# Optimization experiments

Measured on AMD Instinct MI355X. Metric: run time of the kernel, lower is better.

## Reference

```python
import jax, jax.numpy as jnp
import numpy as np

# Static multi-scale feature map shapes (value_spatial_shapes) - constants for jit.
SPATIAL = [(128, 128), (64, 64), (32, 32), (16, 16)]
D = 256      # embed_dim
NH = 8       # num_heads
HD = D // NH # head_dim = 32
L = 4        # num_levels
P = 4        # num_points
TP = NH * L * P  # 128 total points


def setup_inputs() -> dict:
    key = jax.random.key(0)
    ks = jax.random.split(key, 10)
    bs, lq = 8, 300
    lv = sum(h * w for h, w in SPATIAL)  # 21760
    s = D ** -0.5
    return {
        "query": jax.random.normal(ks[0], (bs, lq, D), jnp.float32),
        "reference_points": jax.random.uniform(ks[1], (bs, lq, L, 4), jnp.float32),
        "value": jax.random.normal(ks[2], (bs, lv, D), jnp.float32),
        "W_value": jax.random.normal(ks[3], (D, D), jnp.float32) * s,
        "b_value": jnp.zeros((D,), jnp.float32),
        "W_off": jax.random.normal(ks[4], (D, TP * 2), jnp.float32) * (s * 0.01),
        "b_off": jax.random.normal(ks[5], (TP * 2,), jnp.float32) * 0.5,
        "W_attn": jax.random.normal(ks[6], (D, TP), jnp.float32) * (s * 0.01),
        "b_attn": jnp.zeros((TP,), jnp.float32),
        "W_out": jax.random.normal(ks[7], (D, D), jnp.float32) * s,
        "b_out": jnp.zeros((D,), jnp.float32),
    }


def _grid_sample(img, grid):
    """torch F.grid_sample(mode='bilinear', padding_mode='zeros', align_corners=False).
    img: [N, C, H, W]; grid: [N, Hg, Wg, 2] in [-1, 1] (x, y). Returns [N, C, Hg, Wg]."""
    N, C, H, W = img.shape
    gx = (grid[..., 0] + 1.0) * (W * 0.5) - 0.5
    gy = (grid[..., 1] + 1.0) * (H * 0.5) - 0.5
    x0f = jnp.floor(gx)
    y0f = jnp.floor(gy)
    x0 = x0f.astype(jnp.int32)
    y0 = y0f.astype(jnp.int32)
    x1, y1 = x0 + 1, y0 + 1
    wx1 = gx - x0f
    wy1 = gy - y0f
    wx0 = 1.0 - wx1
    wy0 = 1.0 - wy1
    imgf = img.reshape(N, C, H * W)

    def gather(ix, iy):
        valid = (ix >= 0) & (ix < W) & (iy >= 0) & (iy < H)
        idx = jnp.clip(iy, 0, H - 1) * W + jnp.clip(ix, 0, W - 1)
        v = jax.vmap(lambda im, ii: im[:, ii])(imgf, idx)  # [N, C, Hg, Wg]
        return v * valid[:, None, :, :].astype(img.dtype)

    return (gather(x0, y0) * (wx0 * wy0)[:, None]
            + gather(x1, y0) * (wx1 * wy0)[:, None]
            + gather(x0, y1) * (wx0 * wy1)[:, None]
            + gather(x1, y1) * (wx1 * wy1)[:, None])


def reference(query, reference_points, value, W_value, b_value, W_off, b_off,
              W_attn, b_attn, W_out, b_out):
    bs, lq, _ = query.shape
    # value projection + head split
    v = (value @ W_value + b_value).reshape(bs, -1, NH, HD)
    # sampling offsets and attention weights from query
    off = (query @ W_off + b_off).reshape(bs, lq, NH, L, P, 2)
    aw = jax.nn.softmax((query @ W_attn + b_attn).reshape(bs, lq, NH, L * P), axis=-1)
    aw = aw.reshape(bs, lq, NH, L, P)
    # reference_points last dim == 4 branch (cx, cy, w, h)
    ref = reference_points  # [bs, lq, L, 4]
    loc = ref[:, :, None, :, None, :2] + off / P * ref[:, :, None, :, None, 2:] * 0.5
    grids = 2.0 * loc - 1.0  # [bs, lq, NH, L, P, 2]
    # split value per level
    splits = np.cumsum([h * w for h, w in SPATIAL])[:-1]
    v_list = jnp.split(v, splits, axis=1)
    samples = []
    for l, (h, w) in enumerate(SPATIAL):
        img = v_list[l].transpose(0, 2, 3, 1).reshape(bs * NH, HD, h, w)
        g = grids[:, :, :, l].transpose(0, 2, 1, 3, 4).reshape(bs * NH, lq, P, 2)
        samples.append(_grid_sample(img, g))  # [bs*NH, HD, lq, P]
    samp = jnp.stack(samples, axis=-2).reshape(bs * NH, HD, lq, L * P)
    awr = aw.transpose(0, 2, 1, 3, 4).reshape(bs * NH, 1, lq, L * P)
    out = (samp * awr).sum(-1).reshape(bs, NH * HD, lq).transpose(0, 2, 1)
    return out @ W_out + b_out
```

## Files before the change

kernel.cpp:

```cpp
#include <hip/hip_runtime.h>
#include <hip/hip_bf16.h>

typedef short bf16x8 __attribute__((ext_vector_type(8)));
typedef unsigned short u16x8 __attribute__((ext_vector_type(8)));
typedef float f32x4 __attribute__((ext_vector_type(4)));

#define LQ 300
#define LV 21760
#define NQ 2400
#define MROWS 174080

#define VBM 32
#define VGRID 512
#define QBLK 38
#define VNT (MROWS / VBM)

__device__ __forceinline__ unsigned short f2bf(float x) {
    __hip_bfloat16 h = __float2bfloat16(x);
    return *reinterpret_cast<unsigned short*>(&h);
}
__device__ __forceinline__ float bf2f(unsigned short s) {
    return __uint_as_float(((unsigned)s) << 16);
}
__device__ __forceinline__ bf16x8 cvt8(float4 a, float4 b) {
    u16x8 u;
    u[0] = f2bf(a.x); u[1] = f2bf(a.y); u[2] = f2bf(a.z); u[3] = f2bf(a.w);
    u[4] = f2bf(b.x); u[5] = f2bf(b.y); u[6] = f2bf(b.z); u[7] = f2bf(b.w);
    return (bf16x8)u;
}
__device__ __forceinline__ bf16x8 cvt8v(f32x4 a, f32x4 b) {
    u16x8 u;
    u[0] = f2bf(a[0]); u[1] = f2bf(a[1]); u[2] = f2bf(a[2]); u[3] = f2bf(a[3]);
    u[4] = f2bf(b[0]); u[5] = f2bf(b[1]); u[6] = f2bf(b[2]); u[7] = f2bf(b[3]);
    return (bf16x8)u;
}

__global__ void k_wt(const float* __restrict__ Wv, const float* __restrict__ Woff,
                     const float* __restrict__ Wattn, const float* __restrict__ Wout,
                     unsigned short* __restrict__ ws) {
    int i = blockIdx.x * 256 + threadIdx.x;
    if (i < 65536) {
        int n = i >> 8, k = i & 255;
        ws[i] = f2bf(Wv[k * 256 + n]);
    } else if (i < 65536 + 98304) {
        int j = i - 65536;
        int n = j >> 8, k = j & 255;
        float s = (n < 256) ? Woff[k * 256 + n] : Wattn[k * 128 + (n - 256)];
        ws[i] = f2bf(s);
    } else {
        int j = i - 163840;
        int n = j >> 8, k = j & 255;
        ws[i] = f2bf(Wout[k * 256 + n]);
    }
}

__global__ __launch_bounds__(256, 2) void k_vgemm(
    const float* __restrict__ A, const unsigned short* __restrict__ Bt,
    const float* __restrict__ bias, unsigned short* __restrict__ V,
    const float* __restrict__ Q, const unsigned short* __restrict__ Woa,
    const float* __restrict__ b_off, const float* __restrict__ b_attn,
    float* __restrict__ offattn)
{
    __shared__ __align__(16) float buf[2][VBM * 256];
    const int t = threadIdx.x;
    const int lane = t & 63;
    const int wv = t >> 6;
    const int fr = lane & 15, kg = lane >> 4;

    if (blockIdx.x < QBLK) {
        const int rowBase = blockIdx.x * 64;
        int rr[4];
#pragma unroll
        for (int m = 0; m < 4; ++m) rr[m] = min(rowBase + m * 16 + fr, NQ - 1);

        f32x4 acc[4][6];
#pragma unroll
        for (int m = 0; m < 4; m++)
#pragma unroll
            for (int n = 0; n < 6; n++) { f32x4 z = {0.f, 0.f, 0.f, 0.f}; acc[m][n] = z; }

#pragma unroll
        for (int kk = 0; kk < 8; ++kk) {
            const int kb = kk * 32 + kg * 8;
            bf16x8 a[4];
#pragma unroll
            for (int m = 0; m < 4; ++m) {
                float4 q0 = *(const float4*)(Q + (size_t)rr[m] * 256 + kb);
                float4 q1 = *(const float4*)(Q + (size_t)rr[m] * 256 + kb + 4);
                a[m] = cvt8(q0, q1);
            }
#pragma unroll
            for (int n = 0; n < 6; n++) {
                bf16x8 bb = *(const bf16x8*)(Woa + (size_t)(wv * 96 + n * 16 + fr) * 256 + kb);
#pragma unroll
                for (int m = 0; m < 4; ++m)
                    acc[m][n] = __builtin_amdgcn_mfma_f32_16x16x32_bf16(a[m], bb, acc[m][n], 0, 0, 0);
            }
        }

#pragma unroll
        for (int m = 0; m < 4; m++) {
#pragma unroll
            for (int n = 0; n < 6; n++) {
                int col = wv * 96 + n * 16 + fr;
                float bvv = (col < 256) ? b_off[col] : b_attn[col - 256];
#pragma unroll
                for (int r = 0; r < 4; r++) {
                    int row = rowBase + m * 16 + kg * 4 + r;
                    if (row < NQ) offattn[(size_t)row * 384 + col] = acc[m][n][r] + bvv;
                }
            }
        }
        return;
    }

    bf16x8 bw[8][4];
#pragma unroll
    for (int kk = 0; kk < 8; ++kk)
#pragma unroll
        for (int n = 0; n < 4; ++n)
            bw[kk][n] = *(const bf16x8*)(Bt + (size_t)(wv * 64 + n * 16 + fr) * 256 + kk * 32 + kg * 8);
    float bv[4];
#pragma unroll
    for (int n = 0; n < 4; ++n) bv[n] = bias[wv * 64 + n * 16 + fr];

#define VSTAGE(tile, cb)                                                                  \
    {                                                                                     \
        const char* tb = (const char*)(A + (size_t)(tile) * (VBM * 256));                 \
        _Pragma("unroll")                                                                 \
        for (int i = 0; i < 8; ++i) {                                                     \
            const int r = wv * 8 + i;                                                     \
            __builtin_amdgcn_global_load_lds(                                             \
                (const __attribute__((address_space(1))) void*)                           \
                    (tb + (size_t)r * 1024 + ((lane * 16) ^ ((r & 7) << 4))),             \
                (__attribute__((address_space(3))) void*)&buf[cb][r * 256], 16, 0, 0);    \
        }                                                                                 \
    }

    const int tb0 = (int)blockIdx.x - QBLK;
    VSTAGE(tb0, 0);

    int cur = 0;
    for (int tile = tb0; tile < VNT; tile += VGRID, cur ^= 1) {
        const int nxt = tile + VGRID;
        const bool stged = (nxt < VNT);
        if (stged) VSTAGE(nxt, cur ^ 1);
        if (tile == tb0) {
            if (stged) asm volatile("s_waitcnt vmcnt(8)" ::: "memory");
            else       asm volatile("s_waitcnt vmcnt(0)" ::: "memory");
        } else {
            if (stged) asm volatile("s_waitcnt vmcnt(12)" ::: "memory");
            else       asm volatile("s_waitcnt vmcnt(4)" ::: "memory");
        }
        __builtin_amdgcn_s_barrier();

        const float* lp = buf[cur];
        f32x4 acc[2][4];
#pragma unroll
        for (int m = 0; m < 2; ++m)
#pragma unroll
            for (int n = 0; n < 4; ++n) { f32x4 z = {0.f, 0.f, 0.f, 0.f}; acc[m][n] = z; }

#pragma unroll
        for (int kk = 0; kk < 8; ++kk) {
            bf16x8 a[2];
#pragma unroll
            for (int m = 0; m < 2; ++m) {
                const int row = m * 16 + fr;
                const int bsw = ((kk * 32 + kg * 8) * 4) ^ ((row & 7) << 4);
                f32x4 af0 = *(const f32x4*)((const char*)(lp + row * 256) + bsw);
                f32x4 af1 = *(const f32x4*)((const char*)(lp + row * 256) + (bsw ^ 16));
                a[m] = cvt8v(af0, af1);
            }
#pragma unroll
            for (int m = 0; m < 2; ++m)
#pragma unroll
                for (int n = 0; n < 4; ++n)
                    acc[m][n] = __builtin_amdgcn_mfma_f32_16x16x32_bf16(a[m], bw[kk][n], acc[m][n], 0, 0, 0);
        }

        __builtin_amdgcn_s_barrier();

        unsigned short* cp = (unsigned short*)buf[cur];
#pragma unroll
        for (int n = 0; n < 4; ++n)
#pragma unroll
            for (int m = 0; m < 2; ++m)
#pragma unroll
                for (int r = 0; r < 4; ++r)
                    cp[(m * 16 + kg * 4 + r) * 264 + wv * 64 + n * 16 + fr] =
                        f2bf(acc[m][n][r] + bv[n]);
        asm volatile("s_waitcnt lgkmcnt(0)" ::: "memory");
        __builtin_amdgcn_sched_barrier(0);
        __builtin_amdgcn_s_barrier();

        unsigned short* ob = V + (size_t)tile * (VBM * 256);
#pragma unroll
        for (int i = 0; i < 4; ++i) {
            const int f = i * 256 + t;
            const int row = f >> 5, col = (f & 31) * 8;
            *(u16x8*)(ob + row * 256 + col) = *(const u16x8*)&cp[row * 264 + col];
        }
        __builtin_amdgcn_s_barrier();
    }
#undef VSTAGE
}

__global__ __launch_bounds__(256) void k_sample(
    const float* __restrict__ refp, const float* __restrict__ offattn,
    const unsigned short* __restrict__ V, const unsigned short* __restrict__ Wout,
    const float* __restrict__ b_out, float* __restrict__ out)
{
    __shared__ float aw[2][128], gx[2][128], gy[2][128];
    __shared__ float att_s[2][256];
    const int t = threadIdx.x;
    const int jj = t >> 7;
    const int tt = t & 127;
    const int row = blockIdx.x * 2 + jj;
    const int b = row / LQ;
    const float* oa = offattn + (size_t)row * 384;

    {
        float logit = oa[256 + tt];
        float m = logit;
        m = fmaxf(m, __shfl_xor(m, 1));
        m = fmaxf(m, __shfl_xor(m, 2));
        m = fmaxf(m, __shfl_xor(m, 4));
        m = fmaxf(m, __shfl_xor(m, 8));
        float e = __expf(logit - m);
        float s = e;
        s += __shfl_xor(s, 1);
        s += __shfl_xor(s, 2);
        s += __shfl_xor(s, 4);
        s += __shfl_xor(s, 8);
        aw[jj][tt] = e / s;
        const int l = (tt >> 2) & 3;
        const float Wl = (l == 0) ? 128.f : (l == 1) ? 64.f : (l == 2) ? 32.f : 16.f;
        float ox = oa[2 * tt], oy = oa[2 * tt + 1];
        const float* rp = refp + ((size_t)row * 4 + l) * 4;
        gx[jj][tt] = (rp[0] + ox * 0.125f * rp[2]) * Wl - 0.5f;
        gy[jj][tt] = (rp[1] + oy * 0.125f * rp[3]) * Wl - 0.5f;
    }
    __syncthreads();

    const int h = tt >> 4;
    const int ch = h * 32 + (tt & 15) * 2;
    float acc0 = 0.f, acc1 = 0.f;
#pragma unroll 4
    for (int p = 0; p < 16; p++) {
        const int l = p >> 2;
        const int Wl = (l == 0) ? 128 : (l == 1) ? 64 : (l == 2) ? 32 : 16;
        const int S  = (l == 0) ? 0 : (l == 1) ? 16384 : (l == 2) ? 20480 : 21504;
        int pt = h * 16 + p;
        float a  = aw[jj][pt];
        float sx = gx[jj][pt], sy = gy[jj][pt];
        float x0f = floorf(sx), y0f = floorf(sy);
        int   x0 = (int)x0f, y0 = (int)y0f;
        float wx1 = sx - x0f, wy1 = sy - y0f;
        float wx0 = 1.f - wx1, wy0 = 1.f - wy1;
        bool vx0 = (unsigned)x0 < (unsigned)Wl;
        bool vx1 = (unsigned)(x0 + 1) < (unsigned)Wl;
        bool vy0 = (unsigned)y0 < (unsigned)Wl;
        bool vy1 = (unsigned)(y0 + 1) < (unsigned)Wl;
        float p00x = 0.f, p00y = 0.f, p01x = 0.f, p01y = 0.f;
        float p10x = 0.f, p10y = 0.f, p11x = 0.f, p11y = 0.f;
        size_t pixBase = (size_t)b * LV + S;
        if (vy0) {
            size_t rb = (pixBase + (size_t)y0 * Wl) * 256 + ch;
            if (vx0) { unsigned u = *(const unsigned*)(V + rb + (size_t)x0 * 256);
                       p00x = bf2f((unsigned short)u); p00y = bf2f((unsigned short)(u >> 16)); }
            if (vx1) { unsigned u = *(const unsigned*)(V + rb + (size_t)x0 * 256 + 256);
                       p01x = bf2f((unsigned short)u); p01y = bf2f((unsigned short)(u >> 16)); }
        }
        if (vy1) {
            size_t rb = (pixBase + (size_t)(y0 + 1) * Wl) * 256 + ch;
            if (vx0) { unsigned u = *(const unsigned*)(V + rb + (size_t)x0 * 256);
                       p10x = bf2f((unsigned short)u); p10y = bf2f((unsigned short)(u >> 16)); }
            if (vx1) { unsigned u = *(const unsigned*)(V + rb + (size_t)x0 * 256 + 256);
                       p11x = bf2f((unsigned short)u); p11y = bf2f((unsigned short)(u >> 16)); }
        }
        acc0 += a * (wy0 * (wx0 * p00x + wx1 * p01x) + wy1 * (wx0 * p10x + wx1 * p11x));
        acc1 += a * (wy0 * (wx0 * p00y + wx1 * p01y) + wy1 * (wx0 * p10y + wx1 * p11y));
    }
    att_s[jj][ch] = acc0;
    att_s[jj][ch + 1] = acc1;
    __syncthreads();

    const size_t r0 = (size_t)blockIdx.x * 2;
    float o0 = b_out[t], o1 = o0;
    const unsigned short* wrow = Wout + (size_t)t * 256;
#pragma unroll 8
    for (int k = 0; k < 256; k += 8) {
        bf16x8 w8 = *(const bf16x8*)(wrow + k);
#pragma unroll
        for (int e = 0; e < 8; ++e) {
            float w = bf2f((unsigned short)w8[e]);
            o0 += att_s[0][k + e] * w;
            o1 += att_s[1][k + e] * w;
        }
    }
    out[r0 * 256 + t] = o0;
    out[(r0 + 1) * 256 + t] = o1;
}

extern "C" void kernel_launch(void* const* d_in, const int* in_sizes, int n_in,
                              void* d_out, int out_size, void* d_ws, size_t ws_size,
                              hipStream_t stream) {
    const float* query   = (const float*)d_in[0];
    const float* refp    = (const float*)d_in[1];
    const float* value   = (const float*)d_in[2];
    const float* W_value = (const float*)d_in[3];
    const float* b_value = (const float*)d_in[4];
    const float* W_off   = (const float*)d_in[5];
    const float* b_off   = (const float*)d_in[6];
    const float* W_attn  = (const float*)d_in[7];
    const float* b_attn  = (const float*)d_in[8];
    const float* W_out   = (const float*)d_in[9];
    const float* b_out   = (const float*)d_in[10];
    float* out = (float*)d_out;

    unsigned short* wsu   = (unsigned short*)d_ws;
    unsigned short* Wt_v  = wsu;
    unsigned short* Wt_oa = Wt_v + 65536;
    unsigned short* Wt_out= Wt_oa + 98304;
    unsigned short* V     = Wt_out + 65536;
    float* offattn = (float*)(V + (size_t)MROWS * 256);

    k_wt<<<896, 256, 0, stream>>>(W_value, W_off, W_attn, W_out, wsu);
    k_vgemm<<<VGRID + QBLK, 256, 0, stream>>>(value, Wt_v, b_value, V,
                                              query, Wt_oa, b_off, b_attn, offattn);
    k_sample<<<NQ / 2, 256, 0, stream>>>(refp, offattn, V, Wt_out, b_out, out);
}
```

Measured before the change: 133.6 us.

## Split query projection into its own kernel and enlarge value-GEMM tiles to 64 rows

The query offset/attention projection moves out of the value-projection kernel into a separate 38-block kernel. The value GEMM now uses 512-thread blocks with 64-row tiles, with eight waves arranged as 2x4 over rows and columns, and a grid of 256. The aim is to remove the imbalance between the mixed query and value blocks and to spread the per-thread weight-register load over more rows. In exchange there is an extra serialized launch, twice the LDS per block (128KB double buffer), which may lower occupancy, and fewer blocks in the grid.

```diff
diff --git a/kernel.cpp b/kernel.cpp
--- a/kernel.cpp
+++ b/kernel.cpp
@@ -10,9 +10,8 @@
 #define NQ 2400
 #define MROWS 174080
 
-#define VBM 32
-#define VGRID 512
-#define QBLK 38
+#define VBM 64
+#define VGRID 256
 #define VNT (MROWS / VBM)
 
 __device__ __forceinline__ unsigned short f2bf(float x) {
@@ -54,75 +53,26 @@
     }
 }
 
-__global__ __launch_bounds__(256, 2) void k_vgemm(
+__global__ __launch_bounds__(512, 2) void k_vgemm(
     const float* __restrict__ A, const unsigned short* __restrict__ Bt,
-    const float* __restrict__ bias, unsigned short* __restrict__ V,
-    const float* __restrict__ Q, const unsigned short* __restrict__ Woa,
-    const float* __restrict__ b_off, const float* __restrict__ b_attn,
-    float* __restrict__ offattn)
+    const float* __restrict__ bias, unsigned short* __restrict__ V)
 {
     __shared__ __align__(16) float buf[2][VBM * 256];
     const int t = threadIdx.x;
     const int lane = t & 63;
     const int wv = t >> 6;
+    const int wr = wv >> 2, wc = wv & 3;
     const int fr = lane & 15, kg = lane >> 4;
 
-    if (blockIdx.x < QBLK) {
-        const int rowBase = blockIdx.x * 64;
-        int rr[4];
-#pragma unroll
-        for (int m = 0; m < 4; ++m) rr[m] = min(rowBase + m * 16 + fr, NQ - 1);
-
-        f32x4 acc[4][6];
-#pragma unroll
-        for (int m = 0; m < 4; m++)
-#pragma unroll
-            for (int n = 0; n < 6; n++) { f32x4 z = {0.f, 0.f, 0.f, 0.f}; acc[m][n] = z; }
-
-#pragma unroll
-        for (int kk = 0; kk < 8; ++kk) {
-            const int kb = kk * 32 + kg * 8;
-            bf16x8 a[4];
-#pragma unroll
-            for (int m = 0; m < 4; ++m) {
-                float4 q0 = *(const float4*)(Q + (size_t)rr[m] * 256 + kb);
-                float4 q1 = *(const float4*)(Q + (size_t)rr[m] * 256 + kb + 4);
-                a[m] = cvt8(q0, q1);
-            }
-#pragma unroll
-            for (int n = 0; n < 6; n++) {
-                bf16x8 bb = *(const bf16x8*)(Woa + (size_t)(wv * 96 + n * 16 + fr) * 256 + kb);
-#pragma unroll
-                for (int m = 0; m < 4; ++m)
-                    acc[m][n] = __builtin_amdgcn_mfma_f32_16x16x32_bf16(a[m], bb, acc[m][n], 0, 0, 0);
-            }
-        }
-
-#pragma unroll
-        for (int m = 0; m < 4; m++) {
-#pragma unroll
-            for (int n = 0; n < 6; n++) {
-                int col = wv * 96 + n * 16 + fr;
-                float bvv = (col < 256) ? b_off[col] : b_attn[col - 256];
-#pragma unroll
-                for (int r = 0; r < 4; r++) {
-                    int row = rowBase + m * 16 + kg * 4 + r;
-                    if (row < NQ) offattn[(size_t)row * 384 + col] = acc[m][n][r] + bvv;
-                }
-            }
-        }
-        return;
-    }
-
     bf16x8 bw[8][4];
 #pragma unroll
     for (int kk = 0; kk < 8; ++kk)
 #pragma unroll
         for (int n = 0; n < 4; ++n)
-            bw[kk][n] = *(const bf16x8*)(Bt + (size_t)(wv * 64 + n * 16 + fr) * 256 + kk * 32 + kg * 8);
+            bw[kk][n] = *(const bf16x8*)(Bt + (size_t)(wc * 64 + n * 16 + fr) * 256 + kk * 32 + kg * 8);
     float bv[4];
 #pragma unroll
-    for (int n = 0; n < 4; ++n) bv[n] = bias[wv * 64 + n * 16 + fr];
+    for (int n = 0; n < 4; ++n) bv[n] = bias[wc * 64 + n * 16 + fr];
 
 #define VSTAGE(tile, cb)                                                                  \
     {                                                                                     \
@@ -137,7 +87,7 @@
         }                                                                                 \
     }
 
-    const int tb0 = (int)blockIdx.x - QBLK;
+    const int tb0 = (int)blockIdx.x;
     VSTAGE(tb0, 0);
 
     int cur = 0;
@@ -166,7 +116,7 @@
             bf16x8 a[2];
 #pragma unroll
             for (int m = 0; m < 2; ++m) {
-                const int row = m * 16 + fr;
+                const int row = wr * 32 + m * 16 + fr;
                 const int bsw = ((kk * 32 + kg * 8) * 4) ^ ((row & 7) << 4);
                 f32x4 af0 = *(const f32x4*)((const char*)(lp + row * 256) + bsw);
                 f32x4 af1 = *(const f32x4*)((const char*)(lp + row * 256) + (bsw ^ 16));
@@ -188,7 +138,7 @@
             for (int m = 0; m < 2; ++m)
 #pragma unroll
                 for (int r = 0; r < 4; ++r)
-                    cp[(m * 16 + kg * 4 + r) * 264 + wv * 64 + n * 16 + fr] =
+                    cp[(wr * 32 + m * 16 + kg * 4 + r) * 264 + wc * 64 + n * 16 + fr] =
                         f2bf(acc[m][n][r] + bv[n]);
         asm volatile("s_waitcnt lgkmcnt(0)" ::: "memory");
         __builtin_amdgcn_sched_barrier(0);
@@ -197,13 +147,66 @@
         unsigned short* ob = V + (size_t)tile * (VBM * 256);
 #pragma unroll
         for (int i = 0; i < 4; ++i) {
-            const int f = i * 256 + t;
+            const int f = i * 512 + t;
             const int row = f >> 5, col = (f & 31) * 8;
             *(u16x8*)(ob + row * 256 + col) = *(const u16x8*)&cp[row * 264 + col];
         }
         __builtin_amdgcn_s_barrier();
     }
 #undef VSTAGE
+}
+
+__global__ __launch_bounds__(512) void k_qproj(
+    const float* __restrict__ Q, const unsigned short* __restrict__ Woa,
+    const float* __restrict__ b_off, const float* __restrict__ b_attn,
+    float* __restrict__ offattn)
+{
+    const int t = threadIdx.x;
+    const int lane = t & 63;
+    const int wid = t >> 6;
+    const int wr = wid >> 2, wc = wid & 3;
+    const int fr = lane & 15, kg = lane >> 4;
+    const int rowBase = blockIdx.x * 64;
+
+    const int r0 = min(rowBase + wr * 32 + fr, NQ - 1);
+    const int r1 = min(rowBase + wr * 32 + 16 + fr, NQ - 1);
+
+    f32x4 acc[2][6];
+#pragma unroll
+    for (int m = 0; m < 2; m++)
+#pragma unroll
+        for (int n = 0; n < 6; n++) { f32x4 z = {0.f, 0.f, 0.f, 0.f}; acc[m][n] = z; }
+
+#pragma unroll
+    for (int kk = 0; kk < 8; ++kk) {
+        const int kb = kk * 32 + kg * 8;
+        float4 q00 = *(const float4*)(Q + (size_t)r0 * 256 + kb);
+        float4 q01 = *(const float4*)(Q + (size_t)r0 * 256 + kb + 4);
+        float4 q10 = *(const float4*)(Q + (size_t)r1 * 256 + kb);
+        float4 q11 = *(const float4*)(Q + (size_t)r1 * 256 + kb + 4);
+        bf16x8 a0 = cvt8(q00, q01);
+        bf16x8 a1 = cvt8(q10, q11);
+#pragma unroll
+        for (int n = 0; n < 6; n++) {
+            bf16x8 bb = *(const bf16x8*)(Woa + (size_t)(wc * 96 + n * 16 + fr) * 256 + kb);
+            acc[0][n] = __builtin_amdgcn_mfma_f32_16x16x32_bf16(a0, bb, acc[0][n], 0, 0, 0);
+            acc[1][n] = __builtin_amdgcn_mfma_f32_16x16x32_bf16(a1, bb, acc[1][n], 0, 0, 0);
+        }
+    }
+
+#pragma unroll
+    for (int m = 0; m < 2; m++) {
+#pragma unroll
+        for (int n = 0; n < 6; n++) {
+            int col = wc * 96 + n * 16 + fr;
+            float bvv = (col < 256) ? b_off[col] : b_attn[col - 256];
+#pragma unroll
+            for (int r = 0; r < 4; r++) {
+                int row = rowBase + wr * 32 + m * 16 + kg * 4 + r;
+                if (row < NQ) offattn[(size_t)row * 384 + col] = acc[m][n][r] + bvv;
+            }
+        }
+    }
 }
 
 __global__ __launch_bounds__(256) void k_sample(
@@ -327,7 +330,7 @@
     float* offattn = (float*)(V + (size_t)MROWS * 256);
 
     k_wt<<<896, 256, 0, stream>>>(W_value, W_off, W_attn, W_out, wsu);
-    k_vgemm<<<VGRID + QBLK, 256, 0, stream>>>(value, Wt_v, b_value, V,
-                                              query, Wt_oa, b_off, b_attn, offattn);
+    k_qproj<<<38, 512, 0, stream>>>(query, Wt_oa, b_off, b_attn, offattn);
+    k_vgemm<<<VGRID, 512, 0, stream>>>(value, Wt_v, b_value, V);
     k_sample<<<NQ / 2, 256, 0, stream>>>(refp, offattn, V, Wt_out, b_out, out);
 }
```

After: 148.2 us. +10.9%, slower.
